# Performance work log

Measured on AMD Instinct MI355X. Metric: run time of the kernel, lower is better.

## Reference

```python
import jax, jax.numpy as jnp
import numpy as np

N_HEADS = 8
FACTOR = 5
N_LAYERS = 2
D_MODEL = 512


def _pos_enc(L, d):
    pos = jnp.arange(L, dtype=jnp.float32)[:, None]
    div = jnp.exp(jnp.arange(0, d, 2, dtype=jnp.float32) * (-np.log(10000.0) / d))
    pe = jnp.zeros((L, d), dtype=jnp.float32)
    pe = pe.at[:, 0::2].set(jnp.sin(pos * div))
    pe = pe.at[:, 1::2].set(jnp.cos(pos * div))
    return pe


def _ln(x, g, b, eps=1e-5):
    mu = x.mean(-1, keepdims=True)
    var = ((x - mu) ** 2).mean(-1, keepdims=True)
    return (x - mu) * jax.lax.rsqrt(var + eps) * g + b


def _token_conv(x, W):
    # x: [B, L, C_in]; W: [d_model, C_in, 3]; circular padding k=3 (Informer TokenEmbedding)
    xt = jnp.transpose(x, (0, 2, 1))
    xt = jnp.concatenate([xt[:, :, -1:], xt, xt[:, :, :1]], axis=-1)
    y = jax.lax.conv_general_dilated(xt, W, (1,), 'VALID', dimension_numbers=('NCH', 'OIH', 'NCH'))
    return jnp.transpose(y, (0, 2, 1))


def _prob_attention(Q, K, V):
    # ProbSparse attention (Informer). Q,K,V: [B,H,L,D]
    B, H, L, D = Q.shape
    ln_L = int(np.ceil(np.log(L)))
    U_part = min(FACTOR * ln_L, L)  # sampled keys per query
    u = min(FACTOR * ln_L, L)       # top queries kept
    idx = jax.random.randint(jax.random.key(42), (L, U_part), 0, L)  # shared across B,H as in torch
    K_sample = K[:, :, idx, :]                                  # [B,H,L,U_part,D]
    QK_sample = jnp.einsum('bhld,bhlud->bhlu', Q, K_sample)
    M = QK_sample.max(-1) - QK_sample.mean(-1)                  # sparsity measure [B,H,L]
    _, M_top = jax.lax.top_k(M, u)                              # [B,H,u]
    Q_reduce = jnp.take_along_axis(Q, M_top[..., None], axis=2) # [B,H,u,D]
    scores = jnp.einsum('bhud,bhld->bhul', Q_reduce, K) / jnp.sqrt(jnp.float32(D))
    attn = jax.nn.softmax(scores, axis=-1)
    ctx = jnp.broadcast_to(V.mean(axis=2, keepdims=True), Q.shape)  # non-selected -> mean(V)
    upd = jnp.einsum('bhul,bhld->bhud', attn, V)
    bi = jnp.arange(B)[:, None, None]
    hi = jnp.arange(H)[None, :, None]
    return ctx.at[bi, hi, M_top].set(upd)                       # scatter selected queries


def reference(x_state_enc, x_enc, x_mark_enc, state_emb_W, token_conv_W, time_W, time_b,
              Wq, bq, Wk, bk, Wv, bv, Wo, bo, ln1_g, ln1_b, ln2_g, ln2_b,
              ffn1_W, ffn1_b, ffn2_W, ffn2_b, norm_g, norm_b):
    B, L = x_state_enc.shape
    dm = D_MODEL
    H = N_HEADS
    dk = dm // H
    # StatePosEmbedding: state emb + token conv emb + time-feature linear + sinusoidal pos
    x = state_emb_W[x_state_enc] + _token_conv(x_enc, token_conv_W) + x_mark_enc @ time_W + time_b + _pos_enc(L, dm)
    for l in range(N_LAYERS):
        q = (x @ Wq[l] + bq[l]).reshape(B, L, H, dk).transpose(0, 2, 1, 3)
        k = (x @ Wk[l] + bk[l]).reshape(B, L, H, dk).transpose(0, 2, 1, 3)
        v = (x @ Wv[l] + bv[l]).reshape(B, L, H, dk).transpose(0, 2, 1, 3)
        ctx = _prob_attention(q, k, v).transpose(0, 2, 1, 3).reshape(B, L, dm)
        x = x + (ctx @ Wo[l] + bo[l])
        x = _ln(x, ln1_g[l], ln1_b[l])
        y = jax.nn.gelu(x @ ffn1_W[l] + ffn1_b[l], approximate=False)
        y = y @ ffn2_W[l] + ffn2_b[l]
        x = _ln(x + y, ln2_g[l], ln2_b[l])
    x = _ln(x, norm_g, norm_b)
    logits = x[:, -1:, :] @ state_emb_W.T  # pred_len = 1
    return logits[:, :, :-1]


def setup_inputs() -> dict:
    key = jax.random.key(0)
    ks = jax.random.split(key, 16)
    B, L, C_IN, MARK = 4, 2048, 7, 4
    NG = 100
    dm, dff, NL = 512, 2048, 2
    s = 0.02
    return {
        'x_state_enc': jax.random.randint(ks[0], (B, L), 0, NG + 1),
        'x_enc': jax.random.normal(ks[1], (B, L, C_IN), dtype=jnp.float32),
        'x_mark_enc': jax.random.normal(ks[2], (B, L, MARK), dtype=jnp.float32),
        'state_emb_W': jax.random.normal(ks[3], (NG + 1, dm), dtype=jnp.float32) * s,
        'token_conv_W': jax.random.normal(ks[4], (dm, C_IN, 3), dtype=jnp.float32) * s,
        'time_W': jax.random.normal(ks[5], (MARK, dm), dtype=jnp.float32) * s,
        'time_b': jnp.zeros((dm,), jnp.float32),
        'Wq': jax.random.normal(ks[6], (NL, dm, dm), dtype=jnp.float32) * s,
        'bq': jnp.zeros((NL, dm), jnp.float32),
        'Wk': jax.random.normal(ks[7], (NL, dm, dm), dtype=jnp.float32) * s,
        'bk': jnp.zeros((NL, dm), jnp.float32),
        'Wv': jax.random.normal(ks[8], (NL, dm, dm), dtype=jnp.float32) * s,
        'bv': jnp.zeros((NL, dm), jnp.float32),
        'Wo': jax.random.normal(ks[9], (NL, dm, dm), dtype=jnp.float32) * s,
        'bo': jnp.zeros((NL, dm), jnp.float32),
        'ln1_g': jnp.ones((NL, dm), jnp.float32),
        'ln1_b': jnp.zeros((NL, dm), jnp.float32),
        'ln2_g': jnp.ones((NL, dm), jnp.float32),
        'ln2_b': jnp.zeros((NL, dm), jnp.float32),
        'ffn1_W': jax.random.normal(ks[10], (NL, dm, dff), dtype=jnp.float32) * s,
        'ffn1_b': jnp.zeros((NL, dff), jnp.float32),
        'ffn2_W': jax.random.normal(ks[11], (NL, dff, dm), dtype=jnp.float32) * s,
        'ffn2_b': jnp.zeros((NL, dm), jnp.float32),
        'norm_g': jnp.ones((dm,), jnp.float32),
        'norm_b': jnp.zeros((dm,), jnp.float32),
    }
```

## Files before the change

kernel.cpp:

```cpp
#include <hip/hip_runtime.h>
#include <hip/hip_bf16.h>

#define L_SEQ 2048
#define NB    4
#define DM    512
#define NH    8
#define DK    64
#define DFF   2048
#define NSAMP 40
#define NGRID 100
#define PARTC 16
#define CKEY  128

typedef __attribute__((ext_vector_type(8))) short bf16x8;
typedef __attribute__((ext_vector_type(4))) float f32x4;

__device__ __forceinline__ unsigned rotl32(unsigned x, unsigned r){ return (x<<r)|(x>>(32u-r)); }
__device__ __forceinline__ float bf2f(ushort u){ return __uint_as_float(((unsigned)u)<<16); }
__device__ __forceinline__ ushort f2bf(float f){
  unsigned u = __float_as_uint(f);
  unsigned r = (u + 0x7fffu + ((u>>16)&1u)) >> 16;
  return (ushort)r;
}
__device__ __forceinline__ unsigned fkey(float f){
  unsigned u = __float_as_uint(f);
  return (u & 0x80000000u) ? ~u : (u | 0x80000000u);
}

__device__ __forceinline__ void threefry2x32(unsigned k0, unsigned k1, unsigned x0, unsigned x1,
                                             unsigned &o0, unsigned &o1){
  unsigned ks0=k0, ks1=k1, ks2=k0^k1^0x1BD11BDAu;
  x0 += ks0; x1 += ks1;
#define RND(r) { x0 += x1; x1 = rotl32(x1, r); x1 ^= x0; }
  RND(13u) RND(15u) RND(26u) RND(6u)   x0+=ks1; x1+=ks2+1u;
  RND(17u) RND(29u) RND(16u) RND(24u)  x0+=ks2; x1+=ks0+2u;
  RND(13u) RND(15u) RND(26u) RND(6u)   x0+=ks0; x1+=ks1+3u;
  RND(17u) RND(29u) RND(16u) RND(24u)  x0+=ks1; x1+=ks2+4u;
  RND(13u) RND(15u) RND(26u) RND(6u)   x0+=ks2; x1+=ks0+5u;
#undef RND
  o0=x0; o1=x1;
}

__global__ __launch_bounds__(256) void k_prep(
    const float* __restrict__ Wq, const float* __restrict__ Wk,
    const float* __restrict__ Wv, const float* __restrict__ Wo,
    const float* __restrict__ f1W, const float* __restrict__ f2W,
    const float* __restrict__ bq, const float* __restrict__ bk, const float* __restrict__ bv,
    ushort* __restrict__ wt, float* __restrict__ bcat, int* __restrict__ sidx)
{
  const size_t F1T=1048576, F2T=2097152, LSTR=3145728;
  int bid = blockIdx.x, t = threadIdx.x;
  if (bid >= 6145){
    int i = (bid-6145)*256 + t;
    const int total = L_SEQ*NSAMP;
    if (i < total){
      unsigned o0, o1;
      threefry2x32(0u, 42u, 0u, (unsigned)(total + i), o0, o1);
      sidx[i] = (int)((o0 ^ o1) & (unsigned)(L_SEQ-1));
    }
    return;
  }
  if (bid == 6144){
    for (int i=t; i<2*1536; i+=256){
      int l = i / 1536, r = i - l*1536;
      float v = (r<512) ? bq[l*DM+r] : (r<1024) ? bk[l*DM+r-512] : bv[l*DM+r-1024];
      bcat[i] = v;
    }
    return;
  }
  int l = bid >= 3072; bid -= l*3072;
  const float* src; ushort* dst; int K, N, tile;
  if (bid < 1024){
    int m = bid >> 8; tile = bid & 255;
    src = (m==0?Wq:m==1?Wk:m==2?Wv:Wo) + (size_t)l*DM*DM;
    dst = wt + (size_t)l*LSTR + (size_t)m*262144; K=DM; N=DM;
  } else if (bid < 2048){
    tile = bid-1024; src = f1W + (size_t)l*DM*DFF; dst = wt + (size_t)l*LSTR + F1T; K=DM; N=DFF;
  } else {
    tile = bid-2048; src = f2W + (size_t)l*DFF*DM; dst = wt + (size_t)l*LSTR + F2T; K=DFF; N=DM;
  }
  int ntn = N/32;
  int n0 = (tile % ntn)*32, k0 = (tile / ntn)*32;
  __shared__ float tl[32][33];
  int r = t >> 5, c = t & 31;
  for (int rr=r; rr<32; rr+=8) tl[rr][c] = src[(size_t)(k0+rr)*N + n0 + c];
  __syncthreads();
  for (int rr=r; rr<32; rr+=8)
    dst[(size_t)(n0+rr)*K + k0 + c] = f2bf(tl[c][rr]);
}

__global__ __launch_bounds__(256) void k_embed(const int* __restrict__ tok,
    const float* __restrict__ x_enc, const float* __restrict__ x_mark,
    const float* __restrict__ embW, const float* __restrict__ convW,
    const float* __restrict__ timeW, const float* __restrict__ timeb,
    float* __restrict__ x, ushort* __restrict__ xb){
  int bl = blockIdx.x; int b = bl >> 11; int l = bl & (L_SEQ-1);
  __shared__ float xin[21];
  __shared__ float xm[4];
  int t = threadIdx.x;
  if (t < 21){
    int tt = t/7, i = t - tt*7;
    int ll = (l + tt - 1) & (L_SEQ-1);
    xin[t] = x_enc[((size_t)b*L_SEQ + ll)*7 + i];
  }
  if (t >= 32 && t < 36) xm[t-32] = x_mark[((size_t)b*L_SEQ + l)*4 + (t-32)];
  __syncthreads();
  int tk = tok[bl];
  #pragma unroll
  for (int rep=0; rep<2; rep++){
    int d = t + rep*256;
    float v = embW[(size_t)tk*DM + d];
    const float* w = convW + (size_t)d*21;
    float cv = 0.f;
    #pragma unroll
    for (int tt=0; tt<3; tt++)
      #pragma unroll
      for (int i=0; i<7; i++)
        cv = fmaf(xin[tt*7+i], w[i*3+tt], cv);
    v += cv;
    float tv = timeb[d];
    #pragma unroll
    for (int m=0; m<4; m++) tv = fmaf(xm[m], timeW[m*DM + d], tv);
    v += tv;
    int j = d >> 1;
    float div = expf((float)(2*j) * (-0.017988946039015984f));
    float ang = (float)l * div;
    v += (d & 1) ? cosf(ang) : sinf(ang);
    x[(size_t)bl*DM + d] = v;
    xb[(size_t)bl*DM + d] = f2bf(v);
  }
}

enum { MG_ADD=0, MG_GELU_BF16=1, MG_QKV=2 };

__global__ __launch_bounds__(256) void k_mgemm(
    const ushort* __restrict__ A, const ushort* __restrict__ Bt,
    const float* __restrict__ bias, float* __restrict__ Cf,
    ushort* __restrict__ Cb, int M, int N, int K, int mode)
{
  __shared__ ushort As[2][64][64];
  __shared__ ushort Bs[2][64][64];
  int tid = threadIdx.x, lane = tid & 63, wid = tid >> 6;
  int nwg = gridDim.x*gridDim.y;
  int id  = blockIdx.y*gridDim.x + blockIdx.x;
  int sid = (id & 7)*(nwg >> 3) + (id >> 3);
  int bx = sid % gridDim.x, by = sid / gridDim.x;
  int m0 = by*64, n0 = bx*64;
  int wr = wid >> 1, wc = wid & 1;
  f32x4 acc[2][2];
  #pragma unroll
  for (int i=0;i<2;i++)
    #pragma unroll
    for(int j=0;j<2;j++) acc[i][j] = (f32x4){0.f,0.f,0.f,0.f};

  auto STAGE = [&](int buf, int k0){
    #pragma unroll
    for (int it=0; it<2; it++){
      int e   = it*256 + tid;
      int row = e >> 3, seg = e & 7;
      int gseg = seg ^ (row & 7);
      __builtin_amdgcn_global_load_lds(
        (const __attribute__((address_space(1))) void*)(A + (size_t)(m0+row)*K + k0 + gseg*8),
        (__attribute__((address_space(3))) void*)(&As[buf][0][0] + (size_t)e*8), 16, 0, 0);
      __builtin_amdgcn_global_load_lds(
        (const __attribute__((address_space(1))) void*)(Bt + (size_t)(n0+row)*K + k0 + gseg*8),
        (__attribute__((address_space(3))) void*)(&Bs[buf][0][0] + (size_t)e*8), 16, 0, 0);
    }
  };

  STAGE(0, 0);
  __syncthreads();
  int cur = 0;
  for (int k0 = 0; k0 < K; k0 += 64){
    if (k0 + 64 < K) STAGE(cur^1, k0+64);
    #pragma unroll
    for (int kk=0; kk<2; kk++){
      bf16x8 af[2], bfv[2];
      int seg = kk*4 + (lane>>4);
      #pragma unroll
      for (int i=0;i<2;i++){
        int row = wr*32 + i*16 + (lane&15);
        af[i]  = *(const bf16x8*)&As[cur][row][(seg ^ (row&7))*8];
      }
      #pragma unroll
      for (int j=0;j<2;j++){
        int row = wc*32 + j*16 + (lane&15);
        bfv[j] = *(const bf16x8*)&Bs[cur][row][(seg ^ (row&7))*8];
      }
      #pragma unroll
      for (int i=0;i<2;i++)
        #pragma unroll
        for (int j=0;j<2;j++)
          acc[i][j] = __builtin_amdgcn_mfma_f32_16x16x32_bf16(af[i], bfv[j], acc[i][j], 0,0,0);
    }
    __syncthreads();
    cur ^= 1;
  }

  int fq = lane >> 4, fr = lane & 15;
  for (int i=0;i<2;i++){
    for (int j=0;j<2;j++){
      #pragma unroll
      for (int jj=0;jj<4;jj++){
        int r = m0 + wr*32 + i*16 + fq*4 + jj;
        int c = n0 + wc*32 + j*16 + fr;
        float v = acc[i][j][jj] + bias[c];
        if (mode == MG_ADD){
          Cf[(size_t)r*N + c] += v;
        } else if (mode == MG_GELU_BF16){
          float g = 0.5f*v*(1.f + erff(v*0.70710678118654752f));
          Cb[(size_t)r*N + c] = f2bf(g);
        } else {
          int b = r >> 11, l = r & (L_SEQ-1), m3 = c >> 9, hh = (c>>6)&7, d = c & 63;
          Cb[(size_t)m3*4194304 + (((size_t)b*NH + hh)*L_SEQ + l)*64 + d] = f2bf(v);
        }
      }
    }
  }
}

__global__ __launch_bounds__(256) void k_vmean1(const ushort* __restrict__ V, float* __restrict__ part){
  int blk = blockIdx.x;
  int bh = blk >> 5, ch = blk & 31;
  int t = threadIdx.x, d = t & 63, c = t >> 6;
  const ushort* Vb = V + (size_t)bh*L_SEQ*DK + (size_t)(ch*64 + c*16)*DK;
  float s = 0.f;
  #pragma unroll
  for (int r=0; r<16; r++) s += bf2f(Vb[r*DK + d]);
  __shared__ float red[256];
  red[t]=s; __syncthreads();
  if (t < 64) part[(size_t)blk*64 + t] = red[t]+red[t+64]+red[t+128]+red[t+192];
}
__global__ __launch_bounds__(64) void k_vmean2(const float* __restrict__ part, float* __restrict__ vmean){
  int bh = blockIdx.x, d = threadIdx.x;
  float s = 0.f;
  #pragma unroll
  for (int ch=0; ch<32; ch++) s += part[(size_t)(bh*32+ch)*64 + d];
  vmean[bh*64+d] = s * (1.f/(float)L_SEQ);
}

__global__ __launch_bounds__(256) void k_mscore(const ushort* __restrict__ Q, const ushort* __restrict__ Km,
    const int* __restrict__ idx, float* __restrict__ M){
  int wid = threadIdx.x >> 6, lane = threadIdx.x & 63;
  int bid = blockIdx.x;
  int xcd = bid & 7, rem = bid >> 3;
  int bh = xcd*4 + (rem & 3);
  int qc = rem >> 2;
  int l = qc*4 + wid;
  int g = (bh << 11) + l;
  int sg = lane >> 3, dg = lane & 7;

  bf16x8 qv = *(const bf16x8*)(Q + (size_t)g*64 + dg*8);
  float qf[8];
  #pragma unroll
  for (int e=0;e<8;e++) qf[e] = bf2f((ushort)qv[e]);

  const int* ir = idx + l*NSAMP;
  int ki[5];
  #pragma unroll
  for (int i=0;i<5;i++) ki[i] = ir[i*8 + sg];
  const ushort* Kb = Km + (size_t)bh*L_SEQ*64;
  bf16x8 kv[5];
  #pragma unroll
  for (int i=0;i<5;i++) kv[i] = *(const bf16x8*)(Kb + (size_t)ki[i]*64 + dg*8);

  float mx = -INFINITY, sm = 0.f;
  #pragma unroll
  for (int i=0;i<5;i++){
    float d = 0.f;
    #pragma unroll
    for (int e=0;e<8;e++) d = fmaf(qf[e], bf2f((ushort)kv[i][e]), d);
    #pragma unroll
    for (int off=1; off<8; off<<=1) d += __shfl_xor(d, off);
    mx = fmaxf(mx, d);
    sm += d;
  }
  #pragma unroll
  for (int off=1; off<64; off<<=1){
    mx = fmaxf(mx, __shfl_xor(mx, off));
    sm += __shfl_xor(sm, off);
  }
  if (lane==0) M[g] = mx - sm * (1.f/(8.f*(float)NSAMP));
}

__global__ __launch_bounds__(64) void k_topk1(const float* __restrict__ M,
                                              unsigned long long* __restrict__ cand){
  int blk = blockIdx.x;
  int bh = blk >> 3, sl = blk & 7;
  int lane = threadIdx.x;
  const float* Mr = M + (size_t)bh*L_SEQ + sl*256;
  unsigned long long k[4];
  #pragma unroll
  for (int s=0; s<4; s++){
    int j = s*64 + lane;
    int gidx = sl*256 + j;
    k[s] = ((unsigned long long)fkey(Mr[j]) << 32) | (unsigned)(~gidx);
  }
  for (int sel=0; sel<NSAMP; sel++){
    unsigned long long best = k[0];
    #pragma unroll
    for (int s=1; s<4; s++) best = (k[s] > best) ? k[s] : best;
    #pragma unroll
    for (int off=1; off<64; off<<=1){
      unsigned long long o = __shfl_xor(best, off);
      best = (o > best) ? o : best;
    }
    #pragma unroll
    for (int s=0; s<4; s++) if (k[s] == best) k[s] = 0ull;
    if (lane == 0) cand[(size_t)blk*NSAMP + sel] = best;
  }
}

__global__ __launch_bounds__(64) void k_topk2(const unsigned long long* __restrict__ cand,
                                              int* __restrict__ Mtop){
  int bh = blockIdx.x, lane = threadIdx.x;
  const unsigned long long* cb = cand + (size_t)bh*8*NSAMP;
  unsigned long long k[5];
  #pragma unroll
  for (int s=0; s<5; s++) k[s] = cb[s*64 + lane];
  for (int sel=0; sel<NSAMP; sel++){
    unsigned long long best = k[0];
    #pragma unroll
    for (int s=1; s<5; s++) best = (k[s] > best) ? k[s] : best;
    #pragma unroll
    for (int off=1; off<64; off<<=1){
      unsigned long long o = __shfl_xor(best, off);
      best = (o > best) ? o : best;
    }
    #pragma unroll
    for (int s=0; s<5; s++) if (k[s] == best) k[s] = 0ull;
    if (lane == 0) Mtop[bh*NSAMP + sel] = (int)(~(unsigned)best & (L_SEQ-1));
  }
}

__global__ __launch_bounds__(256) void k_ctxfill(const float* __restrict__ vmean, ushort* __restrict__ ctx){
  int i = blockIdx.x*256 + threadIdx.x;
  int c = i & (DM-1);
  int b = i >> 20;
  int h = c >> 6, d = c & 63;
  ctx[i] = f2bf(vmean[((b<<3)+h)*64 + d]);
}

__global__ __launch_bounds__(256) void k_attn1(const ushort* __restrict__ Q, const ushort* __restrict__ K,
    const ushort* __restrict__ V, const int* __restrict__ Mtop,
    float* __restrict__ pm, float* __restrict__ ps, float* __restrict__ pO){
  int bid = blockIdx.x;
  int xcd = bid & 7, idx = bid >> 3;
  int bh = xcd*4 + (idx & 3), ch = idx >> 2;
  int l0 = ch * CKEY;
  int t = threadIdx.x, lane = t & 63, w = t >> 6;

  __shared__ ushort Qs[48][64];
  __shared__ ushort Ks[CKEY][64];
  __shared__ ushort Vs[CKEY][66];
  __shared__ ushort Ps[48][136];
  __shared__ float rmax[4][48];
  __shared__ float rsum[4][48];
  __shared__ float Oacc[48][64];
  __shared__ int qidx[48];

  if (t < 40) qidx[t] = Mtop[bh*NSAMP + t];
  const ushort* Kb = K + ((size_t)bh*L_SEQ + l0)*64;
  #pragma unroll
  for (int i=0;i<4;i++){
    int e = i*256 + t;
    __builtin_amdgcn_global_load_lds(
      (const __attribute__((address_space(1))) void*)(Kb + (size_t)e*8),
      (__attribute__((address_space(3))) void*)(&Ks[0][0] + (size_t)e*8), 16, 0, 0);
  }
  __syncthreads();

  const ushort* Qb = Q + (size_t)bh*L_SEQ*64;
  {
    int row = t >> 3, seg = t & 7;
    bf16x8 qv = *(const bf16x8*)(Qb + (size_t)qidx[row]*64 + seg*8);
    *(bf16x8*)&Qs[row][seg*8] = qv;
    if (t < 128){
      int r2 = 32 + (t>>3);
      bf16x8 z = (bf16x8){0,0,0,0,0,0,0,0};
      if (r2 < 40) z = *(const bf16x8*)(Qb + (size_t)qidx[r2]*64 + (t&7)*8);
      *(bf16x8*)&Qs[r2][(t&7)*8] = z;
    }
  }
  const ushort* Vb = V + ((size_t)bh*L_SEQ + l0)*64;
  #pragma unroll
  for (int i=0;i<4;i++){
    int e = i*256 + t;
    int row = e >> 3, seg = e & 7;
    bf16x8 vv = *(const bf16x8*)(Vb + (size_t)e*8);
    *(bf16x8*)&Vs[row][seg*8] = vv;
  }
  __syncthreads();

  for (int i=t; i<48*64; i+=256) ((float*)Oacc)[i] = 0.f;

  f32x4 sa[3][2];
  #pragma unroll
  for (int i=0;i<3;i++) for (int j=0;j<2;j++) sa[i][j] = (f32x4){0.f,0.f,0.f,0.f};
  #pragma unroll
  for (int ks=0; ks<2; ks++){
    int ko = ks*32 + (lane>>4)*8;
    bf16x8 af[3], bf[2];
    #pragma unroll
    for (int i=0;i<3;i++) af[i] = *(const bf16x8*)&Qs[i*16 + (lane&15)][ko];
    #pragma unroll
    for (int j=0;j<2;j++) bf[j] = *(const bf16x8*)&Ks[w*32 + j*16 + (lane&15)][ko];
    #pragma unroll
    for (int i=0;i<3;i++)
      #pragma unroll
      for (int j=0;j<2;j++)
        sa[i][j] = __builtin_amdgcn_mfma_f32_16x16x32_bf16(af[i], bf[j], sa[i][j], 0,0,0);
  }
  #pragma unroll
  for (int i=0;i<3;i++)
    #pragma unroll
    for (int j=0;j<2;j++)
      #pragma unroll
      for (int jj=0;jj<4;jj++) sa[i][j][jj] *= 0.125f;
  #pragma unroll
  for (int i=0;i<3;i++){
    #pragma unroll
    for (int jj=0;jj<4;jj++){
      float mx = fmaxf(sa[i][0][jj], sa[i][1][jj]);
      #pragma unroll
      for (int off=1; off<16; off<<=1) mx = fmaxf(mx, __shfl_xor(mx, off));
      if ((lane&15)==0) rmax[w][i*16 + (lane>>4)*4 + jj] = mx;
    }
  }
  __syncthreads();
  #pragma unroll
  for (int i=0;i<3;i++){
    #pragma unroll
    for (int jj=0;jj<4;jj++){
      int row = i*16 + (lane>>4)*4 + jj;
      float m = fmaxf(fmaxf(rmax[0][row], rmax[1][row]), fmaxf(rmax[2][row], rmax[3][row]));
      float p0 = __expf(sa[i][0][jj] - m);
      float p1 = __expf(sa[i][1][jj] - m);
      Ps[row][w*32 + (lane&15)]      = f2bf(p0);
      Ps[row][w*32 + 16 + (lane&15)] = f2bf(p1);
      float sm = p0 + p1;
      #pragma unroll
      for (int off=1; off<16; off<<=1) sm += __shfl_xor(sm, off);
      if ((lane&15)==0) rsum[w][row] = sm;
    }
  }
  __syncthreads();

  f32x4 oa[3][4];
  #pragma unroll
  for (int i=0;i<3;i++) for (int j=0;j<4;j++) oa[i][j] = (f32x4){0.f,0.f,0.f,0.f};
  {
    bf16x8 pa[3], vb[4];
    int kbase = w*32 + (lane>>4)*8;
    #pragma unroll
    for (int i=0;i<3;i++) pa[i] = *(const bf16x8*)&Ps[i*16 + (lane&15)][kbase];
    #pragma unroll
    for (int j=0;j<4;j++){
      #pragma unroll
      for (int e=0;e<8;e++) vb[j][e] = (short)Vs[kbase + e][j*16 + (lane&15)];
    }
    #pragma unroll
    for (int i=0;i<3;i++)
      #pragma unroll
      for (int j=0;j<4;j++)
        oa[i][j] = __builtin_amdgcn_mfma_f32_16x16x32_bf16(pa[i], vb[j], oa[i][j], 0,0,0);
  }
  #pragma unroll
  for (int ww=0; ww<4; ww++){
    if (w == ww){
      #pragma unroll
      for (int i=0;i<3;i++)
        #pragma unroll
        for (int j=0;j<4;j++)
          #pragma unroll
          for (int jj=0;jj<4;jj++)
            Oacc[i*16 + (lane>>4)*4 + jj][j*16 + (lane&15)] += oa[i][j][jj];
    }
    __syncthreads();
  }

  size_t base = ((size_t)bh*PARTC + ch);
  if (t < 40){
    float m = fmaxf(fmaxf(rmax[0][t], rmax[1][t]), fmaxf(rmax[2][t], rmax[3][t]));
    pm[base*40 + t] = m;
    ps[base*40 + t] = rsum[0][t]+rsum[1][t]+rsum[2][t]+rsum[3][t];
  }
  {
    int row = t >> 3, d0 = (t&7)*8;
    float* dst = pO + (base*48 + row)*64 + d0;
    #pragma unroll
    for (int e=0;e<8;e++) dst[e] = Oacc[row][d0+e];
    if (t < 64){
      int r2 = 32 + (t>>3);
      float* dst2 = pO + (base*48 + r2)*64 + d0;
      #pragma unroll
      for (int e=0;e<8;e++) dst2[e] = Oacc[r2][d0+e];
    }
  }
}

__global__ __launch_bounds__(256) void k_attn2(const float* __restrict__ pm, const float* __restrict__ ps,
    const float* __restrict__ pO, const int* __restrict__ Mtop, ushort* __restrict__ ctx){
  int bh = blockIdx.x, b = bh >> 3, h = bh & 7;
  int t = threadIdx.x;
  __shared__ float wch[PARTC][40];
  __shared__ float inv_s[40];
  __shared__ int qidx[40];
  if (t < 40){
    qidx[t] = Mtop[bh*NSAMP + t];
    float m = -INFINITY;
    #pragma unroll
    for (int c=0;c<PARTC;c++) m = fmaxf(m, pm[((size_t)bh*PARTC + c)*40 + t]);
    float s = 0.f;
    #pragma unroll
    for (int c=0;c<PARTC;c++){
      float wc = __expf(pm[((size_t)bh*PARTC + c)*40 + t] - m);
      wch[c][t] = wc;
      s += wc * ps[((size_t)bh*PARTC + c)*40 + t];
    }
    inv_s[t] = 1.f / s;
  }
  __syncthreads();
  #pragma unroll
  for (int iter=0; iter<2; iter++){
    int row = iter*32 + (t>>3);
    if (row < 40){
      int d0 = (t&7)*8;
      float o[8] = {0.f,0.f,0.f,0.f,0.f,0.f,0.f,0.f};
      for (int c=0;c<PARTC;c++){
        const float* pp = pO + (((size_t)bh*PARTC + c)*48 + row)*64 + d0;
        float wc = wch[c][row];
        float4 a = *(const float4*)pp, b4 = *(const float4*)(pp+4);
        o[0]=fmaf(wc,a.x,o[0]); o[1]=fmaf(wc,a.y,o[1]); o[2]=fmaf(wc,a.z,o[2]); o[3]=fmaf(wc,a.w,o[3]);
        o[4]=fmaf(wc,b4.x,o[4]); o[5]=fmaf(wc,b4.y,o[5]); o[6]=fmaf(wc,b4.z,o[6]); o[7]=fmaf(wc,b4.w,o[7]);
      }
      float is = inv_s[row];
      bf16x8 wv;
      #pragma unroll
      for (int e=0;e<8;e++) wv[e] = (short)f2bf(o[e]*is);
      *(bf16x8*)(ctx + ((size_t)b*L_SEQ + qidx[row])*DM + h*64 + d0) = wv;
    }
  }
}

__global__ __launch_bounds__(256) void k_ln(float* __restrict__ x,
    const float* __restrict__ g, const float* __restrict__ b,
    ushort* __restrict__ xb){
  int row = blockIdx.x*4 + (threadIdx.x>>6);
  int lane = threadIdx.x & 63;
  float* xr = x + (size_t)row*DM + lane*8;
  float4 v0 = *(const float4*)(xr);
  float4 v1 = *(const float4*)(xr + 4);
  float s = v0.x+v0.y+v0.z+v0.w+v1.x+v1.y+v1.z+v1.w;
  #pragma unroll
  for (int off=1; off<64; off<<=1) s += __shfl_xor(s, off);
  float mu = s * (1.f/(float)DM);
  float d0=v0.x-mu, d1=v0.y-mu, d2=v0.z-mu, d3=v0.w-mu;
  float d4=v1.x-mu, d5=v1.y-mu, d6=v1.z-mu, d7=v1.w-mu;
  float q = d0*d0+d1*d1+d2*d2+d3*d3+d4*d4+d5*d5+d6*d6+d7*d7;
  #pragma unroll
  for (int off=1; off<64; off<<=1) q += __shfl_xor(q, off);
  float r = rsqrtf(q * (1.f/(float)DM) + 1e-5f);
  float4 g0 = *(const float4*)(g + lane*8);
  float4 g1 = *(const float4*)(g + lane*8 + 4);
  float4 b0 = *(const float4*)(b + lane*8);
  float4 b1 = *(const float4*)(b + lane*8 + 4);
  float o0=d0*r*g0.x+b0.x, o1=d1*r*g0.y+b0.y, o2=d2*r*g0.z+b0.z, o3=d3*r*g0.w+b0.w;
  float o4=d4*r*g1.x+b1.x, o5=d5*r*g1.y+b1.y, o6=d6*r*g1.z+b1.z, o7=d7*r*g1.w+b1.w;
  *(float4*)(xr)     = (float4){o0,o1,o2,o3};
  *(float4*)(xr + 4) = (float4){o4,o5,o6,o7};
  if (xb){
    bf16x8 w;
    w[0]=(short)f2bf(o0); w[1]=(short)f2bf(o1); w[2]=(short)f2bf(o2); w[3]=(short)f2bf(o3);
    w[4]=(short)f2bf(o4); w[5]=(short)f2bf(o5); w[6]=(short)f2bf(o6); w[7]=(short)f2bf(o7);
    *(bf16x8*)(xb + (size_t)row*DM + lane*8) = w;
  }
}

__global__ __launch_bounds__(64) void k_logits(const float* __restrict__ x, const float* __restrict__ embW,
                                               float* __restrict__ out){
  int bid = blockIdx.x;
  int b = bid / NGRID, g = bid - b*NGRID;
  const float* xr = x + ((size_t)b*L_SEQ + (L_SEQ-1))*DM;
  const float* er = embW + (size_t)g*DM;
  int lane = threadIdx.x;
  float s = 0.f;
  for (int d=lane; d<DM; d+=64) s = fmaf(xr[d], er[d], s);
  for (int off=32; off; off>>=1) s += __shfl_xor(s, off);
  if (lane==0) out[bid] = s;
}

extern "C" void kernel_launch(void* const* d_in, const int* in_sizes, int n_in,
                              void* d_out, int out_size, void* d_ws, size_t ws_size,
                              hipStream_t stream) {
  const int*   tok    = (const int*)d_in[0];
  const float* x_enc  = (const float*)d_in[1];
  const float* x_mark = (const float*)d_in[2];
  const float* embW   = (const float*)d_in[3];
  const float* convW  = (const float*)d_in[4];
  const float* timeW  = (const float*)d_in[5];
  const float* timeb  = (const float*)d_in[6];
  const float* Wq = (const float*)d_in[7];  const float* bq = (const float*)d_in[8];
  const float* Wk = (const float*)d_in[9];  const float* bk = (const float*)d_in[10];
  const float* Wv = (const float*)d_in[11]; const float* bv = (const float*)d_in[12];
  const float* Wo = (const float*)d_in[13]; const float* bo = (const float*)d_in[14];
  const float* ln1g = (const float*)d_in[15]; const float* ln1b = (const float*)d_in[16];
  const float* ln2g = (const float*)d_in[17]; const float* ln2b = (const float*)d_in[18];
  const float* f1W = (const float*)d_in[19]; const float* f1b = (const float*)d_in[20];
  const float* f2W = (const float*)d_in[21]; const float* f2b = (const float*)d_in[22];
  const float* nrmg = (const float*)d_in[23]; const float* nrmb = (const float*)d_in[24];
  float* out = (float*)d_out;

  char* ws = (char*)d_ws;
  float*  x    = (float*) (ws);
  ushort* xb   = (ushort*)(ws + ((size_t)16<<20));
  ushort* q    = (ushort*)(ws + ((size_t)24<<20));
  ushort* kbuf = (ushort*)(ws + ((size_t)32<<20));
  ushort* vbuf = (ushort*)(ws + ((size_t)40<<20));
  ushort* ctx  = (ushort*)(ws + ((size_t)48<<20));
  ushort* hbuf = (ushort*)(ws + ((size_t)24<<20));
  ushort* wt   = (ushort*)(ws + ((size_t)56<<20));
  float*  Mbuf = (float*) (ws + ((size_t)69<<20));
  int*    Mtop = (int*)   (ws + ((size_t)70<<20));
  int*    sidx = (int*)   (ws + ((size_t)71<<20));
  float*  vmean= (float*) (ws + ((size_t)72<<20));
  float*  bcat = (float*) (ws + ((size_t)73<<20));
  float*  part = (float*) (ws + ((size_t)74<<20));
  float*  pO   = (float*) (ws + ((size_t)75<<20));
  float*  pmb  = (float*) (ws + ((size_t)82<<20));
  float*  psb  = (float*) (ws + ((size_t)82<<20) + 102400);
  unsigned long long* cand = (unsigned long long*)(ws + ((size_t)83<<20));

  const int Mrows = NB*L_SEQ;
  const size_t WQT=0, WOT=786432, F1T=1048576, F2T=2097152, LSTR=3145728;

  k_prep<<<6465, 256, 0, stream>>>(Wq, Wk, Wv, Wo, f1W, f2W, bq, bk, bv, wt, bcat, sidx);
  k_embed<<<NB*L_SEQ, 256, 0, stream>>>(tok, x_enc, x_mark, embW, convW, timeW, timeb, x, xb);

  for (int l=0; l<2; l++){
    size_t b5 = (size_t)l*DM;
    ushort* wl = wt + (size_t)l*LSTR;

    k_mgemm<<<dim3(1536/64, Mrows/64), 256, 0, stream>>>(xb, wl+WQT, bcat+l*1536, nullptr, q, Mrows, 1536, DM, MG_QKV);
    k_vmean1<<<NB*NH*32, 256, 0, stream>>>(vbuf, part);
    k_vmean2<<<NB*NH, 64, 0, stream>>>(part, vmean);
    k_mscore<<<NB*NH*L_SEQ/4, 256, 0, stream>>>(q, kbuf, sidx, Mbuf);
    k_topk1<<<NB*NH*8, 64, 0, stream>>>(Mbuf, cand);
    k_topk2<<<NB*NH, 64, 0, stream>>>(cand, Mtop);
    k_ctxfill<<<(NB*L_SEQ*DM)/256, 256, 0, stream>>>(vmean, ctx);
    k_attn1<<<NB*NH*PARTC, 256, 0, stream>>>(q, kbuf, vbuf, Mtop, pmb, psb, pO);
    k_attn2<<<NB*NH, 256, 0, stream>>>(pmb, psb, pO, Mtop, ctx);
    k_mgemm<<<dim3(DM/64, Mrows/64), 256, 0, stream>>>(ctx, wl+WOT, bo+b5, x, nullptr, Mrows, DM, DM, MG_ADD);
    k_ln<<<Mrows/4, 256, 0, stream>>>(x, ln1g+b5, ln1b+b5, xb);
    k_mgemm<<<dim3(DFF/64, Mrows/64), 256, 0, stream>>>(xb, wl+F1T, f1b + (size_t)l*DFF, nullptr, hbuf, Mrows, DFF, DM, MG_GELU_BF16);
    k_mgemm<<<dim3(DM/64, Mrows/64), 256, 0, stream>>>(hbuf, wl+F2T, f2b+b5, x, nullptr, Mrows, DM, DFF, MG_ADD);
    k_ln<<<Mrows/4, 256, 0, stream>>>(x, ln2g+b5, ln2b+b5, xb);
  }
  k_ln<<<Mrows/4, 256, 0, stream>>>(x, nrmg, nrmb, nullptr);
  k_logits<<<NB*NGRID, 64, 0, stream>>>(x, embW, out);
}
```

Measured before the change: 497.8 us.

## Replace full output projection with per-batch base plus sparse delta updates

Since most context rows equal the per-head mean of V, the output projection of those rows is identical per batch. The new code computes that projection once per batch (ybase) and adds it inside LayerNorm, and for the 40 selected queries per head projects only the difference from the mean and atomically adds it into the residual. This removes the context fill kernel and the full 8192x512x512 Wo GEMM. The cost is a small per-batch matvec, float atomics into x (which makes summation order nondeterministic), and a large shared-memory staging of Wo in attn2.

```diff
diff --git a/kernel.cpp b/kernel.cpp
--- a/kernel.cpp
+++ b/kernel.cpp
@@ -239,6 +239,25 @@
   vmean[bh*64+d] = s * (1.f/(float)L_SEQ);
 }
 
+__global__ __launch_bounds__(256) void k_ybase(const float* __restrict__ vmean,
+    const ushort* __restrict__ WoT, const float* __restrict__ bo, float* __restrict__ ybase){
+  int b = blockIdx.x, t = threadIdx.x;
+  __shared__ float vb[DM];
+  for (int i=t; i<DM; i+=256) vb[i] = vmean[b*DM + i];
+  __syncthreads();
+  for (int n=t; n<DM; n+=256){
+    const ushort* wr = WoT + (size_t)n*DM;
+    float s = bo[n];
+    #pragma unroll
+    for (int k8=0; k8<64; k8++){
+      bf16x8 wv = *(const bf16x8*)(wr + k8*8);
+      #pragma unroll
+      for (int e=0;e<8;e++) s = fmaf(vb[k8*8+e], bf2f((ushort)wv[e]), s);
+    }
+    ybase[b*DM + n] = s;
+  }
+}
+
 __global__ __launch_bounds__(256) void k_mscore(const ushort* __restrict__ Q, const ushort* __restrict__ Km,
     const int* __restrict__ idx, float* __restrict__ M){
   int wid = threadIdx.x >> 6, lane = threadIdx.x & 63;
@@ -333,14 +352,6 @@
   }
 }
 
-__global__ __launch_bounds__(256) void k_ctxfill(const float* __restrict__ vmean, ushort* __restrict__ ctx){
-  int i = blockIdx.x*256 + threadIdx.x;
-  int c = i & (DM-1);
-  int b = i >> 20;
-  int h = c >> 6, d = c & 63;
-  ctx[i] = f2bf(vmean[((b<<3)+h)*64 + d]);
-}
-
 __global__ __launch_bounds__(256) void k_attn1(const ushort* __restrict__ Q, const ushort* __restrict__ K,
     const ushort* __restrict__ V, const int* __restrict__ Mtop,
     float* __restrict__ pm, float* __restrict__ ps, float* __restrict__ pO){
@@ -500,12 +511,17 @@
 }
 
 __global__ __launch_bounds__(256) void k_attn2(const float* __restrict__ pm, const float* __restrict__ ps,
-    const float* __restrict__ pO, const int* __restrict__ Mtop, ushort* __restrict__ ctx){
+    const float* __restrict__ pO, const int* __restrict__ Mtop, const float* __restrict__ vmean,
+    const ushort* __restrict__ WoT, float* __restrict__ x){
   int bh = blockIdx.x, b = bh >> 3, h = bh & 7;
   int t = threadIdx.x;
   __shared__ float wch[PARTC][40];
   __shared__ float inv_s[40];
   __shared__ int qidx[40];
+  __shared__ float vmn[64];
+  __shared__ float dv[40][64];
+  __shared__ ushort Ws[512][64];
+  if (t < 64) vmn[t] = vmean[bh*64 + t];
   if (t < 40){
     qidx[t] = Mtop[bh*NSAMP + t];
     float m = -INFINITY;
@@ -519,6 +535,13 @@
       s += wc * ps[((size_t)bh*PARTC + c)*40 + t];
     }
     inv_s[t] = 1.f / s;
+  }
+  #pragma unroll
+  for (int i=0;i<16;i++){
+    int e = i*256 + t;
+    int n = e >> 3, seg = e & 7;
+    bf16x8 wv = *(const bf16x8*)(WoT + (size_t)n*DM + h*64 + seg*8);
+    *(bf16x8*)&Ws[n][(seg ^ (n&7))*8] = wv;
   }
   __syncthreads();
   #pragma unroll
@@ -535,22 +558,39 @@
         o[4]=fmaf(wc,b4.x,o[4]); o[5]=fmaf(wc,b4.y,o[5]); o[6]=fmaf(wc,b4.z,o[6]); o[7]=fmaf(wc,b4.w,o[7]);
       }
       float is = inv_s[row];
-      bf16x8 wv;
-      #pragma unroll
-      for (int e=0;e<8;e++) wv[e] = (short)f2bf(o[e]*is);
-      *(bf16x8*)(ctx + ((size_t)b*L_SEQ + qidx[row])*DM + h*64 + d0) = wv;
-    }
+      #pragma unroll
+      for (int e=0;e<8;e++) dv[row][d0+e] = o[e]*is - vmn[d0+e];
+    }
+  }
+  __syncthreads();
+  for (int o_=0; o_<80; ++o_){
+    int oi = o_*256 + t;
+    int row = oi >> 9, n = oi & 511;
+    float s = 0.f;
+    #pragma unroll
+    for (int k8=0; k8<8; k8++){
+      bf16x8 wv = *(const bf16x8*)&Ws[n][(k8 ^ (n&7))*8];
+      #pragma unroll
+      for (int e=0;e<8;e++) s = fmaf(dv[row][k8*8+e], bf2f((ushort)wv[e]), s);
+    }
+    atomicAdd(&x[((size_t)b*L_SEQ + qidx[row])*DM + n], s);
   }
 }
 
 __global__ __launch_bounds__(256) void k_ln(float* __restrict__ x,
     const float* __restrict__ g, const float* __restrict__ b,
-    ushort* __restrict__ xb){
+    ushort* __restrict__ xb, const float* __restrict__ yb){
   int row = blockIdx.x*4 + (threadIdx.x>>6);
   int lane = threadIdx.x & 63;
   float* xr = x + (size_t)row*DM + lane*8;
   float4 v0 = *(const float4*)(xr);
   float4 v1 = *(const float4*)(xr + 4);
+  if (yb){
+    const float* yr = yb + (size_t)(row>>11)*DM + lane*8;
+    float4 y0 = *(const float4*)(yr), y1 = *(const float4*)(yr+4);
+    v0.x+=y0.x; v0.y+=y0.y; v0.z+=y0.z; v0.w+=y0.w;
+    v1.x+=y1.x; v1.y+=y1.y; v1.z+=y1.z; v1.w+=y1.w;
+  }
   float s = v0.x+v0.y+v0.z+v0.w+v1.x+v1.y+v1.z+v1.w;
   #pragma unroll
   for (int off=1; off<64; off<<=1) s += __shfl_xor(s, off);
@@ -617,7 +657,6 @@
   ushort* q    = (ushort*)(ws + ((size_t)24<<20));
   ushort* kbuf = (ushort*)(ws + ((size_t)32<<20));
   ushort* vbuf = (ushort*)(ws + ((size_t)40<<20));
-  ushort* ctx  = (ushort*)(ws + ((size_t)48<<20));
   ushort* hbuf = (ushort*)(ws + ((size_t)24<<20));
   ushort* wt   = (ushort*)(ws + ((size_t)56<<20));
   float*  Mbuf = (float*) (ws + ((size_t)69<<20));
@@ -630,6 +669,7 @@
   float*  pmb  = (float*) (ws + ((size_t)82<<20));
   float*  psb  = (float*) (ws + ((size_t)82<<20) + 102400);
   unsigned long long* cand = (unsigned long long*)(ws + ((size_t)83<<20));
+  float*  ybase= (float*) (ws + ((size_t)84<<20));
 
   const int Mrows = NB*L_SEQ;
   const size_t WQT=0, WOT=786432, F1T=1048576, F2T=2097152, LSTR=3145728;
@@ -644,18 +684,17 @@
     k_mgemm<<<dim3(1536/64, Mrows/64), 256, 0, stream>>>(xb, wl+WQT, bcat+l*1536, nullptr, q, Mrows, 1536, DM, MG_QKV);
     k_vmean1<<<NB*NH*32, 256, 0, stream>>>(vbuf, part);
     k_vmean2<<<NB*NH, 64, 0, stream>>>(part, vmean);
+    k_ybase<<<NB, 256, 0, stream>>>(vmean, wl+WOT, bo+b5, ybase);
     k_mscore<<<NB*NH*L_SEQ/4, 256, 0, stream>>>(q, kbuf, sidx, Mbuf);
     k_topk1<<<NB*NH*8, 64, 0, stream>>>(Mbuf, cand);
     k_topk2<<<NB*NH, 64, 0, stream>>>(cand, Mtop);
-    k_ctxfill<<<(NB*L_SEQ*DM)/256, 256, 0, stream>>>(vmean, ctx);
     k_attn1<<<NB*NH*PARTC, 256, 0, stream>>>(q, kbuf, vbuf, Mtop, pmb, psb, pO);
-    k_attn2<<<NB*NH, 256, 0, stream>>>(pmb, psb, pO, Mtop, ctx);
-    k_mgemm<<<dim3(DM/64, Mrows/64), 256, 0, stream>>>(ctx, wl+WOT, bo+b5, x, nullptr, Mrows, DM, DM, MG_ADD);
-    k_ln<<<Mrows/4, 256, 0, stream>>>(x, ln1g+b5, ln1b+b5, xb);
+    k_attn2<<<NB*NH, 256, 0, stream>>>(pmb, psb, pO, Mtop, vmean, wl+WOT, x);
+    k_ln<<<Mrows/4, 256, 0, stream>>>(x, ln1g+b5, ln1b+b5, xb, ybase);
     k_mgemm<<<dim3(DFF/64, Mrows/64), 256, 0, stream>>>(xb, wl+F1T, f1b + (size_t)l*DFF, nullptr, hbuf, Mrows, DFF, DM, MG_GELU_BF16);
     k_mgemm<<<dim3(DM/64, Mrows/64), 256, 0, stream>>>(hbuf, wl+F2T, f2b+b5, x, nullptr, Mrows, DM, DFF, MG_ADD);
-    k_ln<<<Mrows/4, 256, 0, stream>>>(x, ln2g+b5, ln2b+b5, xb);
-  }
-  k_ln<<<Mrows/4, 256, 0, stream>>>(x, nrmg, nrmb, nullptr);
+    k_ln<<<Mrows/4, 256, 0, stream>>>(x, ln2g+b5, ln2b+b5, xb, nullptr);
+  }
+  k_ln<<<Mrows/4, 256, 0, stream>>>(x, nrmg, nrmb, nullptr, nullptr);
   k_logits<<<NB*NGRID, 64, 0, stream>>>(x, embW, out);
 }
```

After: 545.2 us. 1.1x slower.
